# Optimization experiments

Measured on AMD Instinct MI355X. Metric: run time of the kernel, lower is better.

The kernel has to match this reference:

```python
import jax, jax.numpy as jnp
import numpy as np
import math

B, S, D, H = 2, 2048, 2048, 16
HD = D // H  # head_dim = 128


def _rope_tables(seq_len, head_dim, theta=10000.0):
    inv = 1.0 / (theta ** (np.arange(0, head_dim, 2, dtype=np.float32) / head_dim))
    t = np.arange(seq_len, dtype=np.float32)
    freqs = np.outer(t, inv)  # [S, HD/2]
    return jnp.asarray(np.cos(freqs)), jnp.asarray(np.sin(freqs))


def setup_inputs() -> dict:
    key = jax.random.key(0)
    ks = jax.random.split(key, 6)
    std = 1.0 / math.sqrt(D)
    x = jax.random.normal(ks[0], (B, S, D), dtype=jnp.float32)
    wq_w = jax.random.normal(ks[1], (D, D), dtype=jnp.float32) * std
    wk_w = jax.random.normal(ks[2], (D, D), dtype=jnp.float32) * std
    wv_w = jax.random.normal(ks[3], (D, D), dtype=jnp.float32) * std
    wo_w = jax.random.normal(ks[4], (D, D), dtype=jnp.float32) * std
    zb = jnp.zeros((D,), dtype=jnp.float32)
    fc, fs = _rope_tables(S, HD)
    return {"x": x, "wq_w": wq_w, "wq_b": zb, "wk_w": wk_w, "wk_b": zb,
            "wv_w": wv_w, "wv_b": zb, "wo_w": wo_w, "wo_b": zb,
            "freqs_cos": fc, "freqs_sin": fs}


def _apply_rope(q, k, cos, sin):
    # q, k: [B, S, H, HD]; cos/sin: [S, HD/2] -> broadcast [1, S, 1, HD/2]
    cos = cos[None, :, None, :]
    sin = sin[None, :, None, :]

    def rot(t):
        tr, ti = t[..., 0::2], t[..., 1::2]
        orr = tr * cos - ti * sin
        oi = tr * sin + ti * cos
        return jnp.stack([orr, oi], axis=-1).reshape(t.shape)

    return rot(q), rot(k)


def reference(x, wq_w, wq_b, wk_w, wk_b, wv_w, wv_b, wo_w, wo_b, freqs_cos, freqs_sin):
    b, s, d = x.shape
    q = (x @ wq_w.T + wq_b).reshape(b, s, H, HD)
    k = (x @ wk_w.T + wk_b).reshape(b, s, H, HD)
    v = (x @ wv_w.T + wv_b).reshape(b, s, H, HD)
    q, k = _apply_rope(q, k, freqs_cos[:s], freqs_sin[:s])
    q = q.transpose(0, 2, 1, 3)  # [B,H,S,HD]
    k = k.transpose(0, 2, 1, 3)
    v = v.transpose(0, 2, 1, 3)
    scale = math.sqrt(HD)
    scores = jnp.einsum('bhqd,bhkd->bhqk', q, k) / scale
    causal = jnp.tril(jnp.ones((s, s), dtype=bool))
    scores = jnp.where(causal[None, None], scores, jnp.float32(-jnp.inf))
    attn = jax.nn.softmax(scores, axis=-1)
    out = jnp.einsum('bhqk,bhkd->bhqd', attn, v)
    out = out.transpose(0, 2, 1, 3).reshape(b, s, d)
    out = out @ wo_w.T + wo_b
    return out, k, v
```

## Files before the change

### kernel.cpp

```cpp
#include <hip/hip_runtime.h>

#define B_  2
#define S_  2048
#define D_  2048
#define H_  16
#define HD_ 128

#define QSCALE 0.1275174319003887f

typedef __attribute__((ext_vector_type(4))) float  f32x4;
typedef __attribute__((ext_vector_type(8))) short  short8;
typedef __attribute__((ext_vector_type(8))) __bf16 bf16x8;
typedef __attribute__((ext_vector_type(4))) float  floatv4;
typedef __attribute__((ext_vector_type(4))) unsigned short ushortv4;

__device__ inline unsigned short f2bf(float f) {
  unsigned int u = __builtin_bit_cast(unsigned int, f);
  u += 0x7fffu + ((u >> 16) & 1u);
  return (unsigned short)(u >> 16);
}

__device__ inline void gld16(void* lds, const void* g) {
  __builtin_amdgcn_global_load_lds(
      (const __attribute__((address_space(1))) unsigned int*)g,
      (__attribute__((address_space(3))) unsigned int*)lds, 16, 0, 0);
}

__device__ inline bf16x8 lds_frag(const unsigned short* p) {
  return __builtin_bit_cast(bf16x8, *(const short8*)p);
}
__device__ inline bf16x8 lds_frag_b(const void* p) {
  return __builtin_bit_cast(bf16x8, *(const short8*)p);
}

__global__ void cvt_all(const float* __restrict__ x,
                        const float* __restrict__ w0, const float* __restrict__ w1,
                        const float* __restrict__ w2, const float* __restrict__ w3,
                        unsigned short* __restrict__ xb,
                        unsigned short* __restrict__ wb0, unsigned short* __restrict__ wb1,
                        unsigned short* __restrict__ wb2, unsigned short* __restrict__ wb3) {
  int i = blockIdx.x * 256 + threadIdx.x;
  const float* s; unsigned short* d; int off;
  if (i < 2097152) { s = x; d = xb; off = i; }
  else {
    int j = i - 2097152;
    int r = j >> 20; off = j & 1048575;
    s = (r == 0) ? w0 : (r == 1) ? w1 : (r == 2) ? w2 : w3;
    d = (r == 0) ? wb0 : (r == 1) ? wb1 : (r == 2) ? wb2 : wb3;
  }
  floatv4 v = ((const floatv4*)s)[off];
  ushortv4 o;
  o.x = f2bf(v.x); o.y = f2bf(v.y); o.z = f2bf(v.z); o.w = f2bf(v.w);
  ((ushortv4*)d)[off] = o;
}

__global__ __launch_bounds__(256, 2)
void gemm_nt(const unsigned short* __restrict__ A,
             const unsigned short* __restrict__ W,
             const float* __restrict__ bias,
             float* __restrict__ C, int M, int N, int K) {
  __shared__ __attribute__((aligned(16))) unsigned short As[128 * 32];
  __shared__ __attribute__((aligned(16))) unsigned short Bs[128 * 32];
  const int t = threadIdx.x;
  const int w = t >> 6, lane = t & 63;
  const int quad = lane >> 4, l16 = lane & 15;
  const int m0 = blockIdx.y * 128, n0 = blockIdx.x * 128;
  const int wm = (w >> 1) * 64, wn = (w & 1) * 64;
  f32x4 acc[4][4] = {};

  for (int k0 = 0; k0 < K; k0 += 32) {
    __syncthreads();
#pragma unroll
    for (int j = 0; j < 2; ++j) {
      int o = (t + 256 * j) * 16;
      int row = o >> 6, cb = o & 63;
      gld16((char*)As + w * 1024 + j * 4096,
            (const char*)(A + (size_t)(m0 + row) * K + k0) + cb);
      gld16((char*)Bs + w * 1024 + j * 4096,
            (const char*)(W + (size_t)(n0 + row) * K + k0) + cb);
    }
    __syncthreads();
    bf16x8 af[4], bfr[4];
#pragma unroll
    for (int i = 0; i < 4; ++i)
      af[i] = lds_frag(As + (wm + i * 16 + l16) * 32 + quad * 8);
#pragma unroll
    for (int j = 0; j < 4; ++j)
      bfr[j] = lds_frag(Bs + (wn + j * 16 + l16) * 32 + quad * 8);
#pragma unroll
    for (int i = 0; i < 4; ++i)
#pragma unroll
      for (int j = 0; j < 4; ++j)
        acc[i][j] = __builtin_amdgcn_mfma_f32_16x16x32_bf16(af[i], bfr[j], acc[i][j], 0, 0, 0);
  }

#pragma unroll
  for (int j = 0; j < 4; ++j) {
    int col = n0 + wn + j * 16 + l16;
    float bv = bias[col];
#pragma unroll
    for (int i = 0; i < 4; ++i)
#pragma unroll
      for (int r = 0; r < 4; ++r) {
        int row = m0 + wm + i * 16 + quad * 4 + r;
        C[(size_t)row * N + col] = acc[i][j][r] + bv;
      }
  }
}

__global__ __launch_bounds__(256, 2)
void gemm_qkv(const unsigned short* __restrict__ A,
              const unsigned short* __restrict__ W,
              const float* __restrict__ b0, const float* __restrict__ b1, const float* __restrict__ b2,
              float* __restrict__ C0, float* __restrict__ C1, float* __restrict__ C2,
              int K) {
  __shared__ __attribute__((aligned(16))) unsigned short As[128 * 32];
  __shared__ __attribute__((aligned(16))) unsigned short Bs[128 * 32];
  const int t = threadIdx.x;
  const int w = t >> 6, lane = t & 63;
  const int quad = lane >> 4, l16 = lane & 15;
  const int m0 = blockIdx.y * 128, n0 = blockIdx.x * 128;
  const int wm = (w >> 1) * 64, wn = (w & 1) * 64;
  f32x4 acc[4][4] = {};

  for (int k0 = 0; k0 < K; k0 += 32) {
    __syncthreads();
#pragma unroll
    for (int j = 0; j < 2; ++j) {
      int o = (t + 256 * j) * 16;
      int row = o >> 6, cb = o & 63;
      gld16((char*)As + w * 1024 + j * 4096,
            (const char*)(A + (size_t)(m0 + row) * K + k0) + cb);
      gld16((char*)Bs + w * 1024 + j * 4096,
            (const char*)(W + (size_t)(n0 + row) * K + k0) + cb);
    }
    __syncthreads();
    bf16x8 af[4], bfr[4];
#pragma unroll
    for (int i = 0; i < 4; ++i)
      af[i] = lds_frag(As + (wm + i * 16 + l16) * 32 + quad * 8);
#pragma unroll
    for (int j = 0; j < 4; ++j)
      bfr[j] = lds_frag(Bs + (wn + j * 16 + l16) * 32 + quad * 8);
#pragma unroll
    for (int i = 0; i < 4; ++i)
#pragma unroll
      for (int j = 0; j < 4; ++j)
        acc[i][j] = __builtin_amdgcn_mfma_f32_16x16x32_bf16(af[i], bfr[j], acc[i][j], 0, 0, 0);
  }

#pragma unroll
  for (int j = 0; j < 4; ++j) {
    int col = n0 + wn + j * 16 + l16;
    int sel = col >> 11;
    const float* bp = (sel == 0) ? b0 : (sel == 1) ? b1 : b2;
    float* Cd      = (sel == 0) ? C0 : (sel == 1) ? C1 : C2;
    int cc = col & 2047;
    float bv = bp[cc];
#pragma unroll
    for (int i = 0; i < 4; ++i)
#pragma unroll
      for (int r = 0; r < 4; ++r) {
        int row = m0 + wm + i * 16 + quad * 4 + r;
        Cd[(size_t)row * 2048 + cc] = acc[i][j][r] + bv;
      }
  }
}

__global__ void rope_kernel(const float* __restrict__ Qbuf,
                            const float* __restrict__ Kbuf,
                            const float* __restrict__ fc,
                            const float* __restrict__ fs,
                            unsigned short* __restrict__ Qa,
                            unsigned short* __restrict__ Ka,
                            float* __restrict__ k_out) {
  int idx = blockIdx.x * 256 + threadIdx.x;
  int i = idx & 63;
  int h = (idx >> 6) & (H_ - 1);
  int s = (idx >> 10) & (S_ - 1);
  int b = idx >> 21;
  size_t src = ((size_t)(b * S_ + s)) * D_ + h * HD_ + 2 * i;
  float2 q = *(const float2*)(Qbuf + src);
  float2 k = *(const float2*)(Kbuf + src);
  float c = fc[s * 64 + i], sn = fs[s * 64 + i];
  float qor = q.x * c - q.y * sn, qoi = q.x * sn + q.y * c;
  float kor = k.x * c - k.y * sn, koi = k.x * sn + k.y * c;
  size_t dst = ((size_t)((b * H_ + h) * S_ + s)) * HD_ + 2 * i;
  *(unsigned int*)(Qa + dst) = (unsigned int)f2bf(qor * QSCALE) | ((unsigned int)f2bf(qoi * QSCALE) << 16);
  *(unsigned int*)(Ka + dst) = (unsigned int)f2bf(kor) | ((unsigned int)f2bf(koi) << 16);
  *(float2*)(k_out + dst) = make_float2(kor, koi);
}

__global__ void vtrans_kernel(const float* __restrict__ Vbuf,
                              float* __restrict__ v_out,
                              unsigned short* __restrict__ Vt) {
  __shared__ float tile[64][33];
  int t = threadIdx.x;
  int s0 = blockIdx.x * 64, d0 = blockIdx.y * 32, bh = blockIdx.z;
  int b = bh >> 4, h = bh & 15;
#pragma unroll
  for (int rr = 0; rr < 8; ++rr) {
    int sl = rr * 8 + (t >> 5), dl = t & 31;
    float v = Vbuf[((size_t)(b * S_ + s0 + sl)) * D_ + h * HD_ + d0 + dl];
    tile[sl][dl] = v;
    v_out[((size_t)(bh * S_ + s0 + sl)) * HD_ + d0 + dl] = v;
  }
  __syncthreads();
#pragma unroll
  for (int rr = 0; rr < 8; ++rr) {
    int dl = rr * 4 + (t >> 6), sl = t & 63;
    Vt[((size_t)(bh * HD_ + d0 + dl)) * S_ + s0 + sl] = f2bf(tile[sl][dl]);
  }
}

__global__ __launch_bounds__(256, 2)
void attn_kernel(const unsigned short* __restrict__ Qa,
                 const unsigned short* __restrict__ Ka,
                 const unsigned short* __restrict__ Vt,
                 unsigned short* __restrict__ Oa) {
  __shared__ __attribute__((aligned(16))) unsigned short Ks[2][64 * 128];
  __shared__ __attribute__((aligned(16))) unsigned short Vs[128 * 64];
  __shared__ __attribute__((aligned(16))) unsigned short Ps[4][16 * 64];
  const int t = threadIdx.x, w = t >> 6, lane = t & 63;
  const int quad = lane >> 4, l16 = lane & 15;
  const int bid = blockIdx.x;
  const int bh = (bid & 7) + 8 * (bid >> 7);
  const int p  = (bid >> 3) & 15;
  const int b = bh >> 4, h = bh & 15;
  const unsigned short* Qp = Qa + (size_t)bh * S_ * HD_;
  const unsigned short* Kp = Ka + (size_t)bh * S_ * HD_;
  const unsigned short* Vp = Vt + (size_t)bh * HD_ * S_;
  const float NEGINF = -__builtin_inff();

  for (int part = 0; part < 2; ++part) {
    const int qs = part ? (31 - p) : p;
    const int q0 = qs * 64;
    const int ntmax = qs;

    __syncthreads();

#pragma unroll
    for (int j = 0; j < 4; ++j) {
      int o = (t + 256 * j) * 16;
      int row = o >> 8, cb = (o & 255) ^ ((row & 7) << 4);
      gld16((char*)Ks[0] + w * 1024 + j * 4096, (const char*)(Kp + (size_t)row * HD_) + cb);
    }
    bf16x8 qf[4];
#pragma unroll
    for (int kk = 0; kk < 4; ++kk)
      qf[kk] = *(const bf16x8*)(Qp + (size_t)(q0 + w * 16 + l16) * HD_ + kk * 32 + quad * 8);

    float m_i[4], l_i[4];
#pragma unroll
    for (int r = 0; r < 4; ++r) { m_i[r] = NEGINF; l_i[r] = 0.f; }
    f32x4 oacc[8] = {};
    int c = 0;

    for (int nt = 0; nt <= ntmax; ++nt) {
      __syncthreads();

#pragma unroll
      for (int j = 0; j < 4; ++j) {
        int o = (t + 256 * j) * 16;
        int vrow = o >> 7, vcb = (o & 127) ^ ((vrow & 7) << 4);
        gld16((char*)Vs + w * 1024 + j * 4096,
              (const char*)(Vp + (size_t)vrow * S_ + nt * 64) + vcb);
      }

      f32x4 sacc[4] = {};
      const char* Kc = (const char*)Ks[c];
#pragma unroll
      for (int j = 0; j < 4; ++j) {
        int krow = j * 16 + l16;
        const char* kbase = Kc + krow * 256;
        int ksw = (krow & 7) << 4;
#pragma unroll
        for (int kk = 0; kk < 4; ++kk) {
          bf16x8 kf = lds_frag_b(kbase + ((kk * 64 + quad * 16) ^ ksw));
          sacc[j] = __builtin_amdgcn_mfma_f32_16x16x32_bf16(qf[kk], kf, sacc[j], 0, 0, 0);
        }
      }

      const bool dotail = (nt == ntmax);
      float rowmax[4], alpha[4], rowsum[4];
#pragma unroll
      for (int r = 0; r < 4; ++r) rowmax[r] = NEGINF;
#pragma unroll
      for (int j = 0; j < 4; ++j) {
        int scol = nt * 64 + j * 16 + l16;
#pragma unroll
        for (int r = 0; r < 4; ++r) {
          float v = sacc[j][r];
          if (dotail && scol > q0 + w * 16 + quad * 4 + r) v = NEGINF;
          sacc[j][r] = v;
          rowmax[r] = fmaxf(rowmax[r], v);
        }
      }
#pragma unroll
      for (int off = 1; off < 16; off <<= 1)
#pragma unroll
        for (int r = 0; r < 4; ++r)
          rowmax[r] = fmaxf(rowmax[r], __shfl_xor(rowmax[r], off));
#pragma unroll
      for (int r = 0; r < 4; ++r) {
        float mnew = fmaxf(m_i[r], rowmax[r]);
        alpha[r] = __builtin_amdgcn_exp2f(m_i[r] - mnew);
        m_i[r] = mnew;
        rowsum[r] = 0.f;
      }
#pragma unroll
      for (int j = 0; j < 4; ++j)
#pragma unroll
        for (int r = 0; r < 4; ++r) {
          float e = __builtin_amdgcn_exp2f(sacc[j][r] - m_i[r]);
          sacc[j][r] = e;
          rowsum[r] += e;
        }
#pragma unroll
      for (int off = 1; off < 16; off <<= 1)
#pragma unroll
        for (int r = 0; r < 4; ++r)
          rowsum[r] += __shfl_xor(rowsum[r], off);
#pragma unroll
      for (int r = 0; r < 4; ++r) l_i[r] = l_i[r] * alpha[r] + rowsum[r];
#pragma unroll
      for (int f = 0; f < 8; ++f)
#pragma unroll
        for (int r = 0; r < 4; ++r) oacc[f][r] *= alpha[r];

      __syncthreads();

      if (nt < ntmax) {
#pragma unroll
        for (int j = 0; j < 4; ++j) {
          int o = (t + 256 * j) * 16;
          int row = o >> 8, cb = (o & 255) ^ ((row & 7) << 4);
          gld16((char*)Ks[c ^ 1] + w * 1024 + j * 4096,
                (const char*)(Kp + (size_t)((nt + 1) * 64 + row) * HD_) + cb);
        }
      }

      char* Pw = (char*)&Ps[w][0];
#pragma unroll
      for (int j = 0; j < 4; ++j)
#pragma unroll
        for (int r = 0; r < 4; ++r) {
          int prow = quad * 4 + r;
          *(unsigned short*)(Pw + prow * 128 + ((2 * (j * 16 + l16)) ^ ((prow & 7) << 4))) = f2bf(sacc[j][r]);
        }
      asm volatile("s_waitcnt lgkmcnt(0)" ::: "memory");

      const char* Vb = (const char*)Vs;
      int psw = (l16 & 7) << 4;
#pragma unroll
      for (int s2 = 0; s2 < 2; ++s2) {
        bf16x8 pf = lds_frag_b(Pw + l16 * 128 + ((s2 * 64 + quad * 16) ^ psw));
#pragma unroll
        for (int f = 0; f < 8; ++f) {
          int vrow = f * 16 + l16;
          bf16x8 vf = lds_frag_b(Vb + vrow * 128 + ((s2 * 64 + quad * 16) ^ ((vrow & 7) << 4)));
          oacc[f] = __builtin_amdgcn_mfma_f32_16x16x32_bf16(pf, vf, oacc[f], 0, 0, 0);
        }
      }
      c ^= 1;
    }

    float invl[4];
#pragma unroll
    for (int r = 0; r < 4; ++r) invl[r] = 1.f / l_i[r];
#pragma unroll
    for (int f = 0; f < 8; ++f)
#pragma unroll
      for (int r = 0; r < 4; ++r) {
        int srow = q0 + w * 16 + quad * 4 + r;
        int d = f * 16 + l16;
        Oa[((size_t)(b * S_ + srow)) * D_ + h * HD_ + d] = f2bf(oacc[f][r] * invl[r]);
      }
  }
}

extern "C" void kernel_launch(void* const* d_in, const int* in_sizes, int n_in,
                              void* d_out, int out_size, void* d_ws, size_t ws_size,
                              hipStream_t stream) {
  const float* x    = (const float*)d_in[0];
  const float* wq_w = (const float*)d_in[1];
  const float* wq_b = (const float*)d_in[2];
  const float* wk_w = (const float*)d_in[3];
  const float* wk_b = (const float*)d_in[4];
  const float* wv_w = (const float*)d_in[5];
  const float* wv_b = (const float*)d_in[6];
  const float* wo_w = (const float*)d_in[7];
  const float* wo_b = (const float*)d_in[8];
  const float* fc   = (const float*)d_in[9];
  const float* fs   = (const float*)d_in[10];

  float* out = (float*)d_out;
  const size_t BSD = (size_t)B_ * S_ * D_;
  float* k_out = out + BSD;
  float* v_out = out + 2 * BSD;

  char* ws = (char*)d_ws;
  unsigned short* xb   = (unsigned short*)(ws);
  unsigned short* wqb  = (unsigned short*)(ws + 16777216);
  unsigned short* wkb  = (unsigned short*)(ws + 25165824);
  unsigned short* wvb  = (unsigned short*)(ws + 33554432);
  unsigned short* wob  = (unsigned short*)(ws + 41943040);
  float*          Vbuf = (float*)(ws + 50331648);
  unsigned short* Qat  = (unsigned short*)(ws + 83886080);
  unsigned short* Kat  = (unsigned short*)(ws + 100663296);
  unsigned short* Vt   = (unsigned short*)(ws + 117440512);
  unsigned short* Ab   = (unsigned short*)(ws + 134217728);

  float* Qbuf = out;
  float* Kbuf = v_out;

  cvt_all<<<24576, 256, 0, stream>>>(x, wq_w, wk_w, wv_w, wo_w, xb, wqb, wkb, wvb, wob);

  gemm_qkv<<<dim3(48, 32), 256, 0, stream>>>(xb, wqb, wq_b, wk_b, wv_b,
                                             Qbuf, Kbuf, Vbuf, 2048);

  rope_kernel<<<16384, 256, 0, stream>>>(Qbuf, Kbuf, fc, fs, Qat, Kat, k_out);
  vtrans_kernel<<<dim3(32, 4, 32), 256, 0, stream>>>(Vbuf, v_out, Vt);
  attn_kernel<<<512, 256, 0, stream>>>(Qat, Kat, Vt, Ab);
  gemm_nt<<<dim3(16, 32), 256, 0, stream>>>(Ab, wob, wo_b, out, 4096, 2048, 2048);
}
```

Measured before the change: 476.3 us.

## Replace QKV GEMM with 8-wave double-buffered pipelined 256x128 tile kernel

Replaces the simple single-buffered QKV projection GEMM with a 512-thread kernel that computes 256x128 tiles over 64-wide K chunks. Global-to-LDS loads into two ping-pong buffers are interleaved with MFMA phases under explicit barriers, waitcnts and setprio. It also applies an XOR swizzle to the LDS layout and remaps workgroups across XCDs. The aim is to hide memory latency and avoid LDS bank conflicts, at the cost of a fragile hand-written schedule and one workgroup per CU.

Result: faster. 451.6 us (-5.2%).

```diff
diff --git a/kernel.cpp b/kernel.cpp
--- a/kernel.cpp
+++ b/kernel.cpp
@@ -108,61 +108,152 @@
   }
 }
 
-__global__ __launch_bounds__(256, 2)
-void gemm_qkv(const unsigned short* __restrict__ A,
-              const unsigned short* __restrict__ W,
-              const float* __restrict__ b0, const float* __restrict__ b1, const float* __restrict__ b2,
-              float* __restrict__ C0, float* __restrict__ C1, float* __restrict__ C2,
-              int K) {
-  __shared__ __attribute__((aligned(16))) unsigned short As[128 * 32];
-  __shared__ __attribute__((aligned(16))) unsigned short Bs[128 * 32];
-  const int t = threadIdx.x;
-  const int w = t >> 6, lane = t & 63;
+template<int MI0, int NJ0>
+__device__ inline void quad_mm(f32x4 (&acc)[4][4], const bf16x8 (&af)[2][2], const bf16x8 (&bf)[2][2]) {
+#pragma unroll
+  for (int mi = 0; mi < 2; ++mi)
+#pragma unroll
+    for (int nj = 0; nj < 2; ++nj)
+#pragma unroll
+      for (int ks = 0; ks < 2; ++ks)
+        acc[MI0 + mi][NJ0 + nj] =
+            __builtin_amdgcn_mfma_f32_16x16x32_bf16(af[mi][ks], bf[nj][ks], acc[MI0 + mi][NJ0 + nj], 0, 0, 0);
+}
+
+__device__ inline void stage(char* ldsbuf, int chunk, const char* gtile, int w, long thrOff) {
+  gld16(ldsbuf + chunk * 8192 + w * 1024, gtile + (long)chunk * 64 * 4096 + thrOff);
+}
+
+#define RDF(dst, buf, baserow)                                                          \
+  do {                                                                                  \
+    int _r0 = (baserow);                                                                \
+    _Pragma("unroll") for (int _ii = 0; _ii < 2; ++_ii) {                               \
+      int _row = _r0 + _ii * 16;                                                        \
+      _Pragma("unroll") for (int _ks = 0; _ks < 2; ++_ks)                               \
+          dst[_ii][_ks] = lds_frag_b((buf) + _row * 128 + ((_ks * 64 + quad * 16) ^ xsw)); \
+    }                                                                                   \
+  } while (0)
+
+#define GBAR() __builtin_amdgcn_s_barrier()
+#define LGK0()                                                 \
+  do {                                                         \
+    asm volatile("s_waitcnt lgkmcnt(0)" ::: "memory");         \
+    __builtin_amdgcn_sched_barrier(0);                         \
+  } while (0)
+
+template<bool QKV>
+__global__ __launch_bounds__(512, 1)
+void gemm8p(const unsigned short* __restrict__ A,
+            const unsigned short* __restrict__ W,
+            const float* __restrict__ b0, const float* __restrict__ b1, const float* __restrict__ b2,
+            float* __restrict__ C0, float* __restrict__ C1, float* __restrict__ C2,
+            int nbx) {
+  __shared__ __attribute__((aligned(16))) char smem[98304];
+  char* As0 = smem;
+  char* As1 = smem + 32768;
+  char* Bs0 = smem + 65536;
+  char* Bs1 = smem + 81920;
+
+  const int t = threadIdx.x, w = t >> 6, lane = t & 63;
   const int quad = lane >> 4, l16 = lane & 15;
-  const int m0 = blockIdx.y * 128, n0 = blockIdx.x * 128;
   const int wm = (w >> 1) * 64, wn = (w & 1) * 64;
+  const int xsw = (l16 & 7) << 4;
+
+  const int nwg = gridDim.x, q8 = nwg >> 3;
+  const int wg = ((int)blockIdx.x & 7) * q8 + ((int)blockIdx.x >> 3);
+  const int by = wg / nbx, bx = wg % nbx;
+  const int m0 = by * 256, n0 = bx * 128;
+
+  const char* Agl = (const char*)A + (size_t)m0 * 4096;
+  const char* Wgl = (const char*)W + (size_t)n0 * 4096;
+  const int sr = t >> 3;
+  const long thrOff = (long)sr * 4096 + (((t & 7) * 16) ^ ((sr & 7) << 4));
+
+#pragma unroll
+  for (int c = 0; c < 4; ++c) stage(As0, c, Agl, w, thrOff);
+#pragma unroll
+  for (int c = 0; c < 2; ++c) stage(Bs0, c, Wgl, w, thrOff);
+#pragma unroll
+  for (int c = 0; c < 4; ++c) stage(As1, c, Agl + 128, w, thrOff);
+#pragma unroll
+  for (int c = 0; c < 2; ++c) stage(Bs1, c, Wgl + 128, w, thrOff);
+  asm volatile("s_waitcnt vmcnt(6)" ::: "memory");
+  GBAR();
+
   f32x4 acc[4][4] = {};
 
-  for (int k0 = 0; k0 < K; k0 += 32) {
-    __syncthreads();
-#pragma unroll
-    for (int j = 0; j < 2; ++j) {
-      int o = (t + 256 * j) * 16;
-      int row = o >> 6, cb = o & 63;
-      gld16((char*)As + w * 1024 + j * 4096,
-            (const char*)(A + (size_t)(m0 + row) * K + k0) + cb);
-      gld16((char*)Bs + w * 1024 + j * 4096,
-            (const char*)(W + (size_t)(n0 + row) * K + k0) + cb);
+  for (int it = 0; it < 16; ++it) {
+    int s0 = 2 * it + 2; if (s0 >= 32) s0 -= 2;
+    int s1 = 2 * it + 3; if (s1 >= 32) s1 -= 2;
+    const char* As0g = Agl + (long)s0 * 128;
+    const char* Bs0g = Wgl + (long)s0 * 128;
+    const char* As1g = Agl + (long)s1 * 128;
+    const char* Bs1g = Wgl + (long)s1 * 128;
+    bf16x8 a01[2][2], a23[2][2], b01[2][2], b23[2][2];
+
+    RDF(a01, As0, wm + l16);
+    RDF(b01, Bs0, wn + l16);
+    GBAR(); LGK0();
+    __builtin_amdgcn_s_setprio(1); quad_mm<0, 0>(acc, a01, b01); __builtin_amdgcn_s_setprio(0);
+    GBAR();
+    RDF(a23, As0, wm + 32 + l16);
+    GBAR(); LGK0();
+    __builtin_amdgcn_s_setprio(1); quad_mm<2, 0>(acc, a23, b01); __builtin_amdgcn_s_setprio(0);
+    GBAR();
+    RDF(b23, Bs0, wn + 32 + l16);
+    stage(As0, 0, As0g, w, thrOff); stage(As0, 1, As0g, w, thrOff);
+    GBAR(); LGK0();
+    __builtin_amdgcn_s_setprio(1); quad_mm<0, 2>(acc, a01, b23); __builtin_amdgcn_s_setprio(0);
+    GBAR();
+    stage(As0, 2, As0g, w, thrOff); stage(As0, 3, As0g, w, thrOff);
+    GBAR(); LGK0();
+    __builtin_amdgcn_s_setprio(1); quad_mm<2, 2>(acc, a23, b23); __builtin_amdgcn_s_setprio(0);
+    asm volatile("s_waitcnt vmcnt(4)" ::: "memory");
+    GBAR();
+    RDF(a01, As1, wm + l16);
+    RDF(b01, Bs1, wn + l16);
+    stage(Bs0, 0, Bs0g, w, thrOff); stage(Bs0, 1, Bs0g, w, thrOff);
+    GBAR(); LGK0();
+    __builtin_amdgcn_s_setprio(1); quad_mm<0, 0>(acc, a01, b01); __builtin_amdgcn_s_setprio(0);
+    GBAR();
+    RDF(a23, As1, wm + 32 + l16);
+    GBAR(); LGK0();
+    __builtin_amdgcn_s_setprio(1); quad_mm<2, 0>(acc, a23, b01); __builtin_amdgcn_s_setprio(0);
+    GBAR();
+    RDF(b23, Bs1, wn + 32 + l16);
+    stage(As1, 0, As1g, w, thrOff); stage(As1, 1, As1g, w, thrOff);
+    GBAR(); LGK0();
+    __builtin_amdgcn_s_setprio(1); quad_mm<0, 2>(acc, a01, b23); __builtin_amdgcn_s_setprio(0);
+    GBAR();
+    stage(As1, 2, As1g, w, thrOff); stage(As1, 3, As1g, w, thrOff);
+    stage(Bs1, 0, Bs1g, w, thrOff); stage(Bs1, 1, Bs1g, w, thrOff);
+    GBAR(); LGK0();
+    __builtin_amdgcn_s_setprio(1); quad_mm<2, 2>(acc, a23, b23); __builtin_amdgcn_s_setprio(0);
+    asm volatile("s_waitcnt vmcnt(6)" ::: "memory");
+    GBAR();
+  }
+
+  asm volatile("s_waitcnt vmcnt(0)" ::: "memory");
+
+#pragma unroll
+  for (int nj = 0; nj < 4; ++nj) {
+    int col = n0 + wn + nj * 16 + l16;
+    const float* bp; float* Cd; int cc;
+    if constexpr (QKV) {
+      int sel = col >> 11;
+      bp = (sel == 0) ? b0 : (sel == 1) ? b1 : b2;
+      Cd = (sel == 0) ? C0 : (sel == 1) ? C1 : C2;
+      cc = col & 2047;
+    } else {
+      bp = b0; Cd = C0; cc = col;
     }
-    __syncthreads();
-    bf16x8 af[4], bfr[4];
-#pragma unroll
-    for (int i = 0; i < 4; ++i)
-      af[i] = lds_frag(As + (wm + i * 16 + l16) * 32 + quad * 8);
-#pragma unroll
-    for (int j = 0; j < 4; ++j)
-      bfr[j] = lds_frag(Bs + (wn + j * 16 + l16) * 32 + quad * 8);
-#pragma unroll
-    for (int i = 0; i < 4; ++i)
-#pragma unroll
-      for (int j = 0; j < 4; ++j)
-        acc[i][j] = __builtin_amdgcn_mfma_f32_16x16x32_bf16(af[i], bfr[j], acc[i][j], 0, 0, 0);
-  }
-
-#pragma unroll
-  for (int j = 0; j < 4; ++j) {
-    int col = n0 + wn + j * 16 + l16;
-    int sel = col >> 11;
-    const float* bp = (sel == 0) ? b0 : (sel == 1) ? b1 : b2;
-    float* Cd      = (sel == 0) ? C0 : (sel == 1) ? C1 : C2;
-    int cc = col & 2047;
     float bv = bp[cc];
 #pragma unroll
-    for (int i = 0; i < 4; ++i)
+    for (int mi = 0; mi < 4; ++mi)
 #pragma unroll
       for (int r = 0; r < 4; ++r) {
-        int row = m0 + wm + i * 16 + quad * 4 + r;
-        Cd[(size_t)row * 2048 + cc] = acc[i][j][r] + bv;
+        int row = m0 + wm + mi * 16 + quad * 4 + r;
+        Cd[(size_t)row * 2048 + cc] = acc[mi][nj][r] + bv;
       }
   }
 }
@@ -416,11 +507,12 @@
 
   cvt_all<<<24576, 256, 0, stream>>>(x, wq_w, wk_w, wv_w, wo_w, xb, wqb, wkb, wvb, wob);
 
-  gemm_qkv<<<dim3(48, 32), 256, 0, stream>>>(xb, wqb, wq_b, wk_b, wv_b,
-                                             Qbuf, Kbuf, Vbuf, 2048);
+  gemm8p<true><<<dim3(768), 512, 0, stream>>>(xb, wqb, wq_b, wk_b, wv_b,
+                                              Qbuf, Kbuf, Vbuf, 48);
 
   rope_kernel<<<16384, 256, 0, stream>>>(Qbuf, Kbuf, fc, fs, Qat, Kat, k_out);
   vtrans_kernel<<<dim3(32, 4, 32), 256, 0, stream>>>(Vbuf, v_out, Vt);
   attn_kernel<<<512, 256, 0, stream>>>(Qat, Kat, Vt, Ab);
+
   gemm_nt<<<dim3(16, 32), 256, 0, stream>>>(Ab, wob, wo_b, out, 4096, 2048, 2048);
 }
```
